# Kernel optimization log

Hardware: AMD Instinct MI355X
Metric: run time of the kernel (lower is better)

The kernel has to match this reference:

```python
import jax, jax.numpy as jnp
import numpy as np

EPS = 1e-5


def setup_inputs() -> dict:
    key = jax.random.key(0)
    ks = jax.random.split(key, 6)
    B, C, H, W, K = 8, 512, 128, 128, 32
    x = jax.random.normal(ks[0], (B, C, H, W), jnp.float32)
    # 1x1 conv projection (ConvModule with BN -> no conv bias)
    conv_w = jax.random.normal(ks[1], (C, C), jnp.float32) * 0.02
    bn2_gamma = jnp.ones((C,), jnp.float32)
    bn2_beta = jnp.zeros((C,), jnp.float32)
    bn2_mean = jnp.zeros((C,), jnp.float32)
    bn2_var = jnp.ones((C,), jnp.float32)
    # Encoding: codewords [K, C], per-code smoothing scale [K]
    codewords = jax.random.normal(ks[2], (K, C), jnp.float32) * 0.1
    scale = -jax.random.uniform(ks[3], (K,), jnp.float32)  # negative scale as in mmcv init
    # BN1d over num_codes
    bn1_gamma = jnp.ones((K,), jnp.float32)
    bn1_beta = jnp.zeros((K,), jnp.float32)
    bn1_mean = jnp.zeros((K,), jnp.float32)
    bn1_var = jnp.ones((K,), jnp.float32)
    # channel-attention fc
    fc_w = jax.random.normal(ks[4], (C, C), jnp.float32) * 0.02
    fc_b = jnp.zeros((C,), jnp.float32)
    return {
        "x": x, "conv_w": conv_w,
        "bn2_gamma": bn2_gamma, "bn2_beta": bn2_beta, "bn2_mean": bn2_mean, "bn2_var": bn2_var,
        "codewords": codewords, "scale": scale,
        "bn1_gamma": bn1_gamma, "bn1_beta": bn1_beta, "bn1_mean": bn1_mean, "bn1_var": bn1_var,
        "fc_w": fc_w, "fc_b": fc_b,
    }


def reference(x, conv_w, bn2_gamma, bn2_beta, bn2_mean, bn2_var,
              codewords, scale, bn1_gamma, bn1_beta, bn1_mean, bn1_var,
              fc_w, fc_b):
    B, C, H, W = x.shape
    K = codewords.shape[0]
    # --- encoding_project: 1x1 conv + BN2d (eval) + ReLU ---
    p = jnp.einsum('bchw,oc->bohw', x, conv_w)
    inv2 = jax.lax.rsqrt(bn2_var + EPS)
    p = (p - bn2_mean[None, :, None, None]) * (inv2 * bn2_gamma)[None, :, None, None] \
        + bn2_beta[None, :, None, None]
    p = jax.nn.relu(p)
    # --- Encoding: scaled-L2 soft assignment + aggregation ---
    feat = p.reshape(B, C, H * W).transpose(0, 2, 1)          # [B, N, C]
    x2 = jnp.sum(feat * feat, axis=-1)                        # [B, N]
    c2 = jnp.sum(codewords * codewords, axis=-1)              # [K]
    xc = jnp.einsum('bnc,kc->bnk', feat, codewords)           # [B, N, K]
    scaled_l2 = scale[None, None, :] * (x2[:, :, None] - 2.0 * xc + c2[None, None, :])
    aw = jax.nn.softmax(scaled_l2, axis=2)                    # [B, N, K]
    # sum_n aw * (feat_n - c_k), without materializing [B,N,K,C]
    enc = jnp.einsum('bnk,bnc->bkc', aw, feat) \
        - jnp.sum(aw, axis=1)[:, :, None] * codewords[None]   # [B, K, C]
    # --- BN1d over codes (eval) + ReLU, then mean over codes ---
    inv1 = jax.lax.rsqrt(bn1_var + EPS)
    enc = (enc - bn1_mean[None, :, None]) * (inv1 * bn1_gamma)[None, :, None] \
        + bn1_beta[None, :, None]
    enc = jax.nn.relu(enc)
    encoding_feat = jnp.mean(enc, axis=1)                     # [B, C]
    # --- sigmoid channel gate + residual multiply-add + ReLU ---
    gamma = jax.nn.sigmoid(encoding_feat @ fc_w.T + fc_b)     # [B, C]
    output = jax.nn.relu(x + x * gamma[:, :, None, None])
    return (encoding_feat, output)
```

## Files before the change

kernel.cpp:

```cpp
#include <hip/hip_runtime.h>
#include <stdint.h>


#define EPSV 1e-5f

constexpr int Bn = 8, Cn = 512, Kn = 32, Nn = 16384;
constexpr int TILE_N = 64;
constexpr int NBLK = 256, BLK_PER_B = NBLK / Bn;
constexpr int TILES_PER_BLK = (Nn / TILE_N) / BLK_PER_B;

typedef float f32x4 __attribute__((ext_vector_type(4)));
typedef __bf16 bf16x8 __attribute__((ext_vector_type(8)));
union U4B8 { uint4 u; bf16x8 b; };

__device__ __forceinline__ uint32_t f2bf(float f) {
  uint32_t u = __float_as_uint(f);
  u += 0x7fffu + ((u >> 16) & 1u);
  return u >> 16;
}
__device__ __forceinline__ float bflo(uint32_t d) { return __uint_as_float(d << 16); }
__device__ __forceinline__ float bfhi(uint32_t d) { return __uint_as_float(d & 0xffff0000u); }

__global__ void k0_prep(const float* __restrict__ conv_w, const float* __restrict__ codewords,
                        const float* __restrict__ g2, const float* __restrict__ b2,
                        const float* __restrict__ m2, const float* __restrict__ v2,
                        uint16_t* __restrict__ WT2, uint16_t* __restrict__ cwb,
                        float* __restrict__ c2, float* __restrict__ bns, float* __restrict__ bnb)
{
  const int idx = blockIdx.x * blockDim.x + threadIdx.x;
  if (idx < Cn * Cn) {
    const int o = idx >> 9, c = idx & 511;
    const int cc = c >> 5, cl = c & 31;
    WT2[((size_t)cc * 512 + o) * 32 + cl] = (uint16_t)f2bf(conv_w[idx]);
  }
  if (idx < Kn * Cn) cwb[idx] = (uint16_t)f2bf(codewords[idx]);
  if (idx < Cn) {
    const float s = g2[idx] * rsqrtf(v2[idx] + EPSV);
    bns[idx] = s;
    bnb[idx] = b2[idx] - m2[idx] * s;
  }
  if (idx < Kn) {
    float s = 0.f;
    for (int c = 0; c < Cn; ++c) { const float v = codewords[idx * 512 + c]; s = fmaf(v, v, s); }
    c2[idx] = s;
  }
}

__launch_bounds__(512, 2)
__global__ void k1_main(const float* __restrict__ x,
                        const uint16_t* __restrict__ WT2,
                        const uint16_t* __restrict__ cwb,
                        const float* __restrict__ bns, const float* __restrict__ bnb,
                        const float* __restrict__ c2g, const float* __restrict__ scaleg,
                        float* __restrict__ encpart, float* __restrict__ awsumpart,
                        int parts)
{
  __shared__ __align__(16) float    sXstage[32][65];
  __shared__ __align__(16) uint16_t sXT[64][40];
  __shared__ __align__(16) uint16_t sF[64][520];
  __shared__ __align__(16) uint16_t sCW[32][520];
  __shared__ __align__(16) float    sAW[64][33];
  __shared__ float sX2[64];
  __shared__ float sBNs[512], sBNb[512];
  __shared__ float sScale[Kn], sC2[Kn];

  const int t    = threadIdx.x;
  const int lane = t & 63, w = t >> 6;
  const int col  = lane & 15, quad = lane >> 4;
  const int b    = blockIdx.x / BLK_PER_B;
  const int tb0  = blockIdx.x % BLK_PER_B;

  {
    const int row = t >> 4, seg = t & 15;
    const uint4* src = (const uint4*)(cwb + row * 512 + seg * 32);
    uint4* dst = (uint4*)&sCW[row][seg * 32];
#pragma unroll
    for (int u = 0; u < 4; ++u) dst[u] = src[u];
    sBNs[t] = bns[t];
    sBNb[t] = bnb[t];
    if (t < Kn) { sScale[t] = scaleg[t]; sC2[t] = c2g[t]; }
  }

  float enc[32];
#pragma unroll
  for (int u = 0; u < 32; ++u) enc[u] = 0.f;
  float awacc = 0.f;
  const int k_e3 = t & 31, cg = t >> 5;

  for (int j = 0; j < TILES_PER_BLK; ++j) {
    const int n0 = (tb0 + j * BLK_PER_B) * TILE_N;

    f32x4 acc[4][4];
#pragma unroll
    for (int ot = 0; ot < 4; ++ot)
#pragma unroll
      for (int nt = 0; nt < 4; ++nt) acc[ot][nt] = (f32x4){0.f, 0.f, 0.f, 0.f};

    uint4 areg[2][4];
    float4 xreg;
    {
      const uint16_t* wp = WT2 + (w * 64 + col) * 32 + quad * 8;
#pragma unroll
      for (int ot = 0; ot < 4; ++ot) areg[0][ot] = *(const uint4*)(wp + ot * 512);
      xreg = *(const float4*)(x + ((size_t)(b * Cn) + (t >> 4)) * Nn + n0 + (t & 15) * 4);
    }

#pragma unroll
    for (int cc = 0; cc < 16; ++cc) {
      const int cur = cc & 1, nxt = cur ^ 1;
      __syncthreads();
      {
        const int c_l = t >> 4, n4 = (t & 15) * 4;
        sXstage[c_l][n4 + 0] = xreg.x;
        sXstage[c_l][n4 + 1] = xreg.y;
        sXstage[c_l][n4 + 2] = xreg.z;
        sXstage[c_l][n4 + 3] = xreg.w;
      }
      __syncthreads();
      {
        const int n = t >> 3, c4 = (t & 7) * 4;
        const float v0 = sXstage[c4 + 0][n], v1 = sXstage[c4 + 1][n];
        const float v2 = sXstage[c4 + 2][n], v3 = sXstage[c4 + 3][n];
        *(uint2*)&sXT[n][c4] = make_uint2(f2bf(v0) | (f2bf(v1) << 16),
                                          f2bf(v2) | (f2bf(v3) << 16));
      }
      if (cc + 1 < 16)
        xreg = *(const float4*)(x + ((size_t)(b * Cn) + (cc + 1) * 32 + (t >> 4)) * Nn + n0 + (t & 15) * 4);
      __syncthreads();
      if (cc + 1 < 16) {
        const uint16_t* wp = WT2 + (size_t)(cc + 1) * 16384 + (w * 64 + col) * 32 + quad * 8;
#pragma unroll
        for (int ot = 0; ot < 4; ++ot) areg[nxt][ot] = *(const uint4*)(wp + ot * 512);
      }
      U4B8 bfr[4];
#pragma unroll
      for (int nt = 0; nt < 4; ++nt) bfr[nt].u = *(const uint4*)&sXT[nt * 16 + col][quad * 8];
#pragma unroll
      for (int ot = 0; ot < 4; ++ot) {
        U4B8 a; a.u = areg[cur][ot];
#pragma unroll
        for (int nt = 0; nt < 4; ++nt)
          acc[ot][nt] = __builtin_amdgcn_mfma_f32_16x16x32_bf16(a.b, bfr[nt].b, acc[ot][nt], 0, 0, 0);
      }
    }

#pragma unroll
    for (int ot = 0; ot < 4; ++ot) {
      const int ob = w * 64 + ot * 16 + quad * 4;
      const float4 s4 = *(const float4*)&sBNs[ob];
      const float4 b4 = *(const float4*)&sBNb[ob];
#pragma unroll
      for (int nt = 0; nt < 4; ++nt) {
        const f32x4 a = acc[ot][nt];
        const float r0 = fmaxf(fmaf(a[0], s4.x, b4.x), 0.f);
        const float r1 = fmaxf(fmaf(a[1], s4.y, b4.y), 0.f);
        const float r2 = fmaxf(fmaf(a[2], s4.z, b4.z), 0.f);
        const float r3 = fmaxf(fmaf(a[3], s4.w, b4.w), 0.f);
        *(uint2*)&sF[nt * 16 + col][ob] = make_uint2(f2bf(r0) | (f2bf(r1) << 16),
                                                     f2bf(r2) | (f2bf(r3) << 16));
      }
    }
    __syncthreads();

    {
      const int n = t >> 3, cb = (t & 7) * 64;
      float s = 0.f;
#pragma unroll
      for (int u = 0; u < 8; ++u) {
        const uint4 d = *(const uint4*)&sF[n][cb + u * 8];
        s = fmaf(bflo(d.x), bflo(d.x), s); s = fmaf(bfhi(d.x), bfhi(d.x), s);
        s = fmaf(bflo(d.y), bflo(d.y), s); s = fmaf(bfhi(d.y), bfhi(d.y), s);
        s = fmaf(bflo(d.z), bflo(d.z), s); s = fmaf(bfhi(d.z), bfhi(d.z), s);
        s = fmaf(bflo(d.w), bflo(d.w), s); s = fmaf(bfhi(d.w), bfhi(d.w), s);
      }
      s += __shfl_xor(s, 1); s += __shfl_xor(s, 2); s += __shfl_xor(s, 4);
      if ((t & 7) == 0) sX2[n] = s;
    }

    {
      const int kt = w & 1, ntl = w >> 1;
      f32x4 xca = (f32x4){0.f, 0.f, 0.f, 0.f};
#pragma unroll
      for (int ks = 0; ks < 16; ++ks) {
        U4B8 af, bf;
        af.u = *(const uint4*)&sCW[kt * 16 + col][ks * 32 + quad * 8];
        bf.u = *(const uint4*)&sF[ntl * 16 + col][ks * 32 + quad * 8];
        xca = __builtin_amdgcn_mfma_f32_16x16x32_bf16(af.b, bf.b, xca, 0, 0, 0);
      }
#pragma unroll
      for (int r = 0; r < 4; ++r)
        sAW[ntl * 16 + col][kt * 16 + quad * 4 + r] = xca[r];
    }
    __syncthreads();

    if (t < 64) {
      const float x2v = sX2[t];
      float m = -1e30f;
#pragma unroll
      for (int k = 0; k < Kn; ++k) {
        const float l = sScale[k] * (x2v - 2.f * sAW[t][k] + sC2[k]);
        sAW[t][k] = l;
        m = fmaxf(m, l);
      }
      float s = 0.f;
#pragma unroll
      for (int k = 0; k < Kn; ++k) { const float e = __expf(sAW[t][k] - m); sAW[t][k] = e; s += e; }
      const float inv = 1.f / s;
#pragma unroll
      for (int k = 0; k < Kn; ++k) sAW[t][k] *= inv;
    }
    __syncthreads();

#pragma unroll 2
    for (int n = 0; n < TILE_N; ++n) {
      const float a = sAW[n][k_e3];
      if (cg == 0) awacc += a;
      const uint16_t* fp = &sF[n][cg * 32];
#pragma unroll
      for (int u = 0; u < 4; ++u) {
        const uint4 d = *(const uint4*)(fp + u * 8);
        enc[u*8+0] = fmaf(a, bflo(d.x), enc[u*8+0]);
        enc[u*8+1] = fmaf(a, bfhi(d.x), enc[u*8+1]);
        enc[u*8+2] = fmaf(a, bflo(d.y), enc[u*8+2]);
        enc[u*8+3] = fmaf(a, bfhi(d.y), enc[u*8+3]);
        enc[u*8+4] = fmaf(a, bflo(d.z), enc[u*8+4]);
        enc[u*8+5] = fmaf(a, bfhi(d.z), enc[u*8+5]);
        enc[u*8+6] = fmaf(a, bflo(d.w), enc[u*8+6]);
        enc[u*8+7] = fmaf(a, bfhi(d.w), enc[u*8+7]);
      }
    }
  }

  if (parts > 1) {
    float* dst = encpart + (((size_t)tb0 * Bn + b) * Kn + k_e3) * Cn + cg * 32;
#pragma unroll
    for (int u = 0; u < 8; ++u)
      *(float4*)(dst + u * 4) = make_float4(enc[u*4+0], enc[u*4+1], enc[u*4+2], enc[u*4+3]);
    if (cg == 0) awsumpart[((size_t)tb0 * Bn + b) * Kn + k_e3] = awacc;
  } else {
    float* dst = encpart + ((size_t)b * Kn + k_e3) * Cn + cg * 32;
#pragma unroll
    for (int u = 0; u < 32; ++u) atomicAdd(dst + u, enc[u]);
    if (cg == 0) atomicAdd(awsumpart + (size_t)b * Kn + k_e3, awacc);
  }
}

__global__ void k2_post(const float* __restrict__ encpart, const float* __restrict__ awsumpart,
                        const float* __restrict__ codewords,
                        const float* __restrict__ g1, const float* __restrict__ b1,
                        const float* __restrict__ m1, const float* __restrict__ v1,
                        const float* __restrict__ fc_w, const float* __restrict__ fc_b,
                        float* __restrict__ ef_out, float* __restrict__ gamma,
                        int parts)
{
  __shared__ float efs[Cn];
  __shared__ float saws[Kn];
  const int b = blockIdx.x, c = threadIdx.x;

  if (c < Kn) {
    float s = 0.f;
    for (int p = 0; p < parts; ++p) s += awsumpart[((size_t)p * Bn + b) * Kn + c];
    saws[c] = s;
  }
  __syncthreads();

  float esum[Kn];
#pragma unroll
  for (int k = 0; k < Kn; ++k) esum[k] = 0.f;
  for (int p = 0; p < parts; ++p) {
    const float* ep = encpart + (((size_t)p * Bn + b) * Kn) * Cn + c;
#pragma unroll
    for (int k = 0; k < Kn; ++k) esum[k] += ep[(size_t)k * Cn];
  }

  float s = 0.f;
#pragma unroll
  for (int k = 0; k < Kn; ++k) {
    float e = esum[k] - saws[k] * codewords[k * Cn + c];
    const float inv = rsqrtf(v1[k] + EPSV);
    e = (e - m1[k]) * (inv * g1[k]) + b1[k];
    s += fmaxf(e, 0.f);
  }
  s *= (1.f / 32.f);
  efs[c] = s;
  ef_out[b * Cn + c] = s;
  __syncthreads();
  const float4* w4 = (const float4*)(fc_w + (size_t)c * Cn);
  const float4* e4 = (const float4*)efs;
  float z = 0.f;
#pragma unroll 8
  for (int i = 0; i < Cn / 4; ++i) {
    const float4 w = w4[i], e = e4[i];
    z = fmaf(w.x, e.x, z); z = fmaf(w.y, e.y, z);
    z = fmaf(w.z, e.z, z); z = fmaf(w.w, e.w, z);
  }
  z += fc_b[c];
  gamma[b * Cn + c] = 1.f / (1.f + __expf(-z));
}

__global__ void k3_out(const float* __restrict__ x, const float* __restrict__ gamma,
                       float* __restrict__ out)
{
  const float4* x4 = (const float4*)x;
  float4* o4 = (float4*)out;
  int i = blockIdx.x * blockDim.x + threadIdx.x;
#pragma unroll
  for (int r = 0; r < 8; ++r, i += 2097152) {
    const int bb = i >> 21;
    const int cc = (i >> 12) & 511;
    const float g = 1.f + gamma[bb * 512 + cc];
    float4 v = x4[i];
    v.x = fmaxf(v.x * g, 0.f);
    v.y = fmaxf(v.y * g, 0.f);
    v.z = fmaxf(v.z * g, 0.f);
    v.w = fmaxf(v.w * g, 0.f);
    o4[i] = v;
  }
}

extern "C" void kernel_launch(void* const* d_in, const int* in_sizes, int n_in,
                              void* d_out, int out_size, void* d_ws, size_t ws_size,
                              hipStream_t stream) {
  const float* x      = (const float*)d_in[0];
  const float* conv_w = (const float*)d_in[1];
  const float* bn2g   = (const float*)d_in[2];
  const float* bn2b   = (const float*)d_in[3];
  const float* bn2m   = (const float*)d_in[4];
  const float* bn2v   = (const float*)d_in[5];
  const float* codew  = (const float*)d_in[6];
  const float* scale  = (const float*)d_in[7];
  const float* bn1g   = (const float*)d_in[8];
  const float* bn1b   = (const float*)d_in[9];
  const float* bn1m   = (const float*)d_in[10];
  const float* bn1v   = (const float*)d_in[11];
  const float* fc_w   = (const float*)d_in[12];
  const float* fc_b   = (const float*)d_in[13];

  const size_t enc_part_bytes = (size_t)BLK_PER_B * Bn * Kn * Cn * 4;
  const size_t aws_part_bytes = (size_t)BLK_PER_B * Bn * Kn * 4;
  const size_t enc_fall_bytes = (size_t)Bn * Kn * Cn * 4;
  const size_t aws_fall_bytes = (size_t)Bn * Kn * 4;
  const size_t fixed_bytes = (size_t)Bn * Cn * 4
                           + (size_t)Cn * Cn * 2
                           + (size_t)Kn * Cn * 2
                           + (size_t)Kn * 4
                           + (size_t)Cn * 4
                           + (size_t)Cn * 4;
  const bool use_parts = ws_size >= enc_part_bytes + aws_part_bytes + fixed_bytes;
  const int parts = use_parts ? BLK_PER_B : 1;
  const size_t enc_bytes = use_parts ? enc_part_bytes : enc_fall_bytes;
  const size_t aws_bytes = use_parts ? aws_part_bytes : aws_fall_bytes;

  char* ws = (char*)d_ws;
  float*    encpart  = (float*)ws;                       ws += enc_bytes;
  float*    awsumpart= (float*)ws;                       ws += aws_bytes;
  float*    gamma    = (float*)ws;                       ws += (size_t)Bn * Cn * 4;
  uint16_t* WT2      = (uint16_t*)ws;                    ws += (size_t)Cn * Cn * 2;
  uint16_t* cwb      = (uint16_t*)ws;                    ws += (size_t)Kn * Cn * 2;
  float*    c2       = (float*)ws;                       ws += (size_t)Kn * 4;
  float*    bns      = (float*)ws;                       ws += (size_t)Cn * 4;
  float*    bnb      = (float*)ws;

  if (!use_parts)
    hipMemsetAsync(encpart, 0, enc_bytes + aws_bytes, stream);

  k0_prep<<<1024, 256, 0, stream>>>(conv_w, codew, bn2g, bn2b, bn2m, bn2v,
                                    WT2, cwb, c2, bns, bnb);
  k1_main<<<NBLK, 512, 0, stream>>>(x, WT2, cwb, bns, bnb, c2, scale,
                                    encpart, awsumpart, parts);
  k2_post<<<Bn, Cn, 0, stream>>>(encpart, awsumpart, codew, bn1g, bn1b, bn1m, bn1v,
                                 fc_w, fc_b, (float*)d_out, gamma, parts);
  k3_out<<<8192, 256, 0, stream>>>(x, gamma, (float*)d_out + Bn * Cn);
}
```

Before: 940.3 us.

## Load full x tile to LDS once per tile, drop per-chunk syncs, add parallel partial reduce

The main kernel now loads the whole 512x64 x tile into LDS as bf16 in a single pass, transposes it into a shared buffer, and runs all 16 k-chunks of the projection MFMA without per-chunk barriers. The same buffer is then reused for the projected features, and codewords are read from global/L1 instead of LDS. A separate reduce kernel sums the per-block partials in parallel instead of k2_post doing it serially over 8 blocks. This trades LDS footprint and the lost overlap of x loads with compute for fewer barriers, and adds an extra kernel launch.

```diff
diff --git a/kernel.cpp b/kernel.cpp
--- a/kernel.cpp
+++ b/kernel.cpp
@@ -55,10 +55,8 @@
                         float* __restrict__ encpart, float* __restrict__ awsumpart,
                         int parts)
 {
-  __shared__ __align__(16) float    sXstage[32][65];
-  __shared__ __align__(16) uint16_t sXT[64][40];
-  __shared__ __align__(16) uint16_t sF[64][520];
-  __shared__ __align__(16) uint16_t sCW[32][520];
+  __shared__ __align__(16) uint32_t sP[512][33];
+  __shared__ __align__(16) uint16_t sXF[64][520];
   __shared__ __align__(16) float    sAW[64][33];
   __shared__ float sX2[64];
   __shared__ float sBNs[512], sBNb[512];
@@ -71,11 +69,6 @@
   const int tb0  = blockIdx.x % BLK_PER_B;
 
   {
-    const int row = t >> 4, seg = t & 15;
-    const uint4* src = (const uint4*)(cwb + row * 512 + seg * 32);
-    uint4* dst = (uint4*)&sCW[row][seg * 32];
-#pragma unroll
-    for (int u = 0; u < 4; ++u) dst[u] = src[u];
     sBNs[t] = bns[t];
     sBNb[t] = bnb[t];
     if (t < Kn) { sScale[t] = scaleg[t]; sC2[t] = c2g[t]; }
@@ -90,59 +83,80 @@
   for (int j = 0; j < TILES_PER_BLK; ++j) {
     const int n0 = (tb0 + j * BLK_PER_B) * TILE_N;
 
+    {
+      const int c0 = t >> 4, n4 = (t & 15) * 4;
+      const float* xp = x + ((size_t)(b * Cn) + c0) * Nn + n0 + n4;
+      const int n2 = n4 >> 1;
+#pragma unroll
+      for (int i = 0; i < 16; ++i) {
+        const float4 v = *(const float4*)(xp + (size_t)i * 32 * Nn);
+        sP[c0 + i * 32][n2 + 0] = f2bf(v.x) | (f2bf(v.y) << 16);
+        sP[c0 + i * 32][n2 + 1] = f2bf(v.z) | (f2bf(v.w) << 16);
+      }
+    }
+    __syncthreads();
+
+    {
+      const int n = t & 63, seg = t >> 6;
+      const int h = (n & 1) * 16, n2 = n >> 1;
+#pragma unroll
+      for (int u = 0; u < 8; ++u) {
+        const int c0 = seg * 64 + u * 8;
+        uint32_t o0, o1, o2, o3;
+        {
+          const uint32_t d0 = sP[c0 + 0][n2], d1 = sP[c0 + 1][n2];
+          o0 = ((d0 >> h) & 0xffffu) | (((d1 >> h) & 0xffffu) << 16);
+        }
+        {
+          const uint32_t d0 = sP[c0 + 2][n2], d1 = sP[c0 + 3][n2];
+          o1 = ((d0 >> h) & 0xffffu) | (((d1 >> h) & 0xffffu) << 16);
+        }
+        {
+          const uint32_t d0 = sP[c0 + 4][n2], d1 = sP[c0 + 5][n2];
+          o2 = ((d0 >> h) & 0xffffu) | (((d1 >> h) & 0xffffu) << 16);
+        }
+        {
+          const uint32_t d0 = sP[c0 + 6][n2], d1 = sP[c0 + 7][n2];
+          o3 = ((d0 >> h) & 0xffffu) | (((d1 >> h) & 0xffffu) << 16);
+        }
+        *(uint4*)&sXF[n][c0] = make_uint4(o0, o1, o2, o3);
+      }
+    }
+    __syncthreads();
+
     f32x4 acc[4][4];
 #pragma unroll
     for (int ot = 0; ot < 4; ++ot)
 #pragma unroll
       for (int nt = 0; nt < 4; ++nt) acc[ot][nt] = (f32x4){0.f, 0.f, 0.f, 0.f};
 
-    uint4 areg[2][4];
-    float4 xreg;
-    {
-      const uint16_t* wp = WT2 + (w * 64 + col) * 32 + quad * 8;
-#pragma unroll
-      for (int ot = 0; ot < 4; ++ot) areg[0][ot] = *(const uint4*)(wp + ot * 512);
-      xreg = *(const float4*)(x + ((size_t)(b * Cn) + (t >> 4)) * Nn + n0 + (t & 15) * 4);
-    }
-
-#pragma unroll
-    for (int cc = 0; cc < 16; ++cc) {
-      const int cur = cc & 1, nxt = cur ^ 1;
-      __syncthreads();
-      {
-        const int c_l = t >> 4, n4 = (t & 15) * 4;
-        sXstage[c_l][n4 + 0] = xreg.x;
-        sXstage[c_l][n4 + 1] = xreg.y;
-        sXstage[c_l][n4 + 2] = xreg.z;
-        sXstage[c_l][n4 + 3] = xreg.w;
-      }
-      __syncthreads();
-      {
-        const int n = t >> 3, c4 = (t & 7) * 4;
-        const float v0 = sXstage[c4 + 0][n], v1 = sXstage[c4 + 1][n];
-        const float v2 = sXstage[c4 + 2][n], v3 = sXstage[c4 + 3][n];
-        *(uint2*)&sXT[n][c4] = make_uint2(f2bf(v0) | (f2bf(v1) << 16),
-                                          f2bf(v2) | (f2bf(v3) << 16));
-      }
-      if (cc + 1 < 16)
-        xreg = *(const float4*)(x + ((size_t)(b * Cn) + (cc + 1) * 32 + (t >> 4)) * Nn + n0 + (t & 15) * 4);
-      __syncthreads();
-      if (cc + 1 < 16) {
-        const uint16_t* wp = WT2 + (size_t)(cc + 1) * 16384 + (w * 64 + col) * 32 + quad * 8;
-#pragma unroll
-        for (int ot = 0; ot < 4; ++ot) areg[nxt][ot] = *(const uint4*)(wp + ot * 512);
-      }
-      U4B8 bfr[4];
-#pragma unroll
-      for (int nt = 0; nt < 4; ++nt) bfr[nt].u = *(const uint4*)&sXT[nt * 16 + col][quad * 8];
-#pragma unroll
-      for (int ot = 0; ot < 4; ++ot) {
-        U4B8 a; a.u = areg[cur][ot];
+    {
+      uint4 areg[2][4];
+      const uint16_t* wbase = WT2 + (w * 64 + col) * 32 + quad * 8;
+#pragma unroll
+      for (int ot = 0; ot < 4; ++ot) areg[0][ot] = *(const uint4*)(wbase + ot * 512);
+#pragma unroll
+      for (int cc = 0; cc < 16; ++cc) {
+        const int cur = cc & 1;
+        if (cc + 1 < 16) {
+          const uint16_t* wp = wbase + (size_t)(cc + 1) * 16384;
+#pragma unroll
+          for (int ot = 0; ot < 4; ++ot) areg[cur ^ 1][ot] = *(const uint4*)(wp + ot * 512);
+        }
+        U4B8 bfr[4];
 #pragma unroll
         for (int nt = 0; nt < 4; ++nt)
-          acc[ot][nt] = __builtin_amdgcn_mfma_f32_16x16x32_bf16(a.b, bfr[nt].b, acc[ot][nt], 0, 0, 0);
-      }
-    }
+          bfr[nt].u = *(const uint4*)&sXF[nt * 16 + col][cc * 32 + quad * 8];
+#pragma unroll
+        for (int ot = 0; ot < 4; ++ot) {
+          U4B8 a; a.u = areg[cur][ot];
+#pragma unroll
+          for (int nt = 0; nt < 4; ++nt)
+            acc[ot][nt] = __builtin_amdgcn_mfma_f32_16x16x32_bf16(a.b, bfr[nt].b, acc[ot][nt], 0, 0, 0);
+        }
+      }
+    }
+    __syncthreads();
 
 #pragma unroll
     for (int ot = 0; ot < 4; ++ot) {
@@ -156,8 +170,8 @@
         const float r1 = fmaxf(fmaf(a[1], s4.y, b4.y), 0.f);
         const float r2 = fmaxf(fmaf(a[2], s4.z, b4.z), 0.f);
         const float r3 = fmaxf(fmaf(a[3], s4.w, b4.w), 0.f);
-        *(uint2*)&sF[nt * 16 + col][ob] = make_uint2(f2bf(r0) | (f2bf(r1) << 16),
-                                                     f2bf(r2) | (f2bf(r3) << 16));
+        *(uint2*)&sXF[nt * 16 + col][ob] = make_uint2(f2bf(r0) | (f2bf(r1) << 16),
+                                                      f2bf(r2) | (f2bf(r3) << 16));
       }
     }
     __syncthreads();
@@ -167,7 +181,7 @@
       float s = 0.f;
 #pragma unroll
       for (int u = 0; u < 8; ++u) {
-        const uint4 d = *(const uint4*)&sF[n][cb + u * 8];
+        const uint4 d = *(const uint4*)&sXF[n][cb + u * 8];
         s = fmaf(bflo(d.x), bflo(d.x), s); s = fmaf(bfhi(d.x), bfhi(d.x), s);
         s = fmaf(bflo(d.y), bflo(d.y), s); s = fmaf(bfhi(d.y), bfhi(d.y), s);
         s = fmaf(bflo(d.z), bflo(d.z), s); s = fmaf(bfhi(d.z), bfhi(d.z), s);
@@ -180,11 +194,12 @@
     {
       const int kt = w & 1, ntl = w >> 1;
       f32x4 xca = (f32x4){0.f, 0.f, 0.f, 0.f};
+      const uint16_t* cwp = cwb + (size_t)(kt * 16 + col) * 512 + quad * 8;
 #pragma unroll
       for (int ks = 0; ks < 16; ++ks) {
         U4B8 af, bf;
-        af.u = *(const uint4*)&sCW[kt * 16 + col][ks * 32 + quad * 8];
-        bf.u = *(const uint4*)&sF[ntl * 16 + col][ks * 32 + quad * 8];
+        af.u = *(const uint4*)(cwp + ks * 32);
+        bf.u = *(const uint4*)&sXF[ntl * 16 + col][ks * 32 + quad * 8];
         xca = __builtin_amdgcn_mfma_f32_16x16x32_bf16(af.b, bf.b, xca, 0, 0, 0);
       }
 #pragma unroll
@@ -215,7 +230,7 @@
     for (int n = 0; n < TILE_N; ++n) {
       const float a = sAW[n][k_e3];
       if (cg == 0) awacc += a;
-      const uint16_t* fp = &sF[n][cg * 32];
+      const uint16_t* fp = &sXF[n][cg * 32];
 #pragma unroll
       for (int u = 0; u < 4; ++u) {
         const uint4 d = *(const uint4*)(fp + u * 8);
@@ -245,6 +260,20 @@
   }
 }
 
+__global__ void k2a_reduce(float* __restrict__ encpart, int parts)
+{
+  const int b = blockIdx.x >> 5, s = blockIdx.x & 31;
+  const int e0 = s * 512 + threadIdx.x;
+#pragma unroll
+  for (int r = 0; r < 2; ++r) {
+    const size_t base = (size_t)b * (Kn * Cn) + e0 + r * 256;
+    float v = encpart[base];
+    for (int p = 1; p < parts; ++p)
+      v += encpart[base + (size_t)p * (Bn * Kn * Cn)];
+    encpart[base] = v;
+  }
+}
+
 __global__ void k2_post(const float* __restrict__ encpart, const float* __restrict__ awsumpart,
                         const float* __restrict__ codewords,
                         const float* __restrict__ g1, const float* __restrict__ b1,
@@ -264,19 +293,10 @@
   }
   __syncthreads();
 
-  float esum[Kn];
-#pragma unroll
-  for (int k = 0; k < Kn; ++k) esum[k] = 0.f;
-  for (int p = 0; p < parts; ++p) {
-    const float* ep = encpart + (((size_t)p * Bn + b) * Kn) * Cn + c;
-#pragma unroll
-    for (int k = 0; k < Kn; ++k) esum[k] += ep[(size_t)k * Cn];
-  }
-
   float s = 0.f;
-#pragma unroll
+#pragma unroll 4
   for (int k = 0; k < Kn; ++k) {
-    float e = esum[k] - saws[k] * codewords[k * Cn + c];
+    float e = encpart[((size_t)b * Kn + k) * Cn + c] - saws[k] * codewords[k * Cn + c];
     const float inv = rsqrtf(v1[k] + EPSV);
     e = (e - m1[k]) * (inv * g1[k]) + b1[k];
     s += fmaxf(e, 0.f);
@@ -368,6 +388,8 @@
                                     WT2, cwb, c2, bns, bnb);
   k1_main<<<NBLK, 512, 0, stream>>>(x, WT2, cwb, bns, bnb, c2, scale,
                                     encpart, awsumpart, parts);
+  if (parts > 1)
+    k2a_reduce<<<256, 256, 0, stream>>>(encpart, parts);
   k2_post<<<Bn, Cn, 0, stream>>>(encpart, awsumpart, codew, bn1g, bn1b, bn1m, bn1v,
                                  fc_w, fc_b, (float*)d_out, gamma, parts);
   k3_out<<<8192, 256, 0, stream>>>(x, gamma, (float*)d_out + Bn * Cn);
```

Measured after the change: 999.1 us. 1.06x slower.
